# Kernel optimization log

Hardware: AMD Instinct MI355X
Metric: run time of the kernel (lower is better)

Reference implementation:

```python
import jax, jax.numpy as jnp
import numpy as np

N = 100000
E = 1600000
H = 128
IN = 16
OUT = 16
L = 3
G = 256  # number of graphs
EPS = 1e-12


def setup_inputs() -> dict:
    key = jax.random.key(0)
    ks = jax.random.split(key, 24)
    s = 0.05
    inp = {
        "x": jax.random.normal(ks[0], (N, IN), jnp.float32),
        "pos": jax.random.normal(ks[1], (N, 3), jnp.float32),
        "edge_index": jax.random.randint(ks[2], (2, E), 0, N, jnp.int64),
        "batch": jnp.sort(jax.random.randint(ks[3], (N,), 0, G, jnp.int64)),
        # node_lin: Linear(IN,H), ReLU, Linear(H,H)
        "node_W1": jax.random.normal(ks[4], (IN, H), jnp.float32) * s,
        "node_b1": jnp.zeros((H,), jnp.float32),
        "node_W2": jax.random.normal(ks[5], (H, H), jnp.float32) * s,
        "node_b2": jnp.zeros((H,), jnp.float32),
        # per-layer local_nn: Linear(H+4,H), ReLU, Linear(H,H)  (stacked over L)
        "local_W1": jax.random.normal(ks[6], (L, H + 4, H), jnp.float32) * s,
        "local_b1": jnp.zeros((L, H), jnp.float32),
        "local_W2": jax.random.normal(ks[7], (L, H, H), jnp.float32) * s,
        "local_b2": jnp.zeros((L, H), jnp.float32),
        # per-layer global_nn: Linear(H,H), ReLU, Linear(H,H)
        "global_W1": jax.random.normal(ks[8], (L, H, H), jnp.float32) * s,
        "global_b1": jnp.zeros((L, H), jnp.float32),
        "global_W2": jax.random.normal(ks[9], (L, H, H), jnp.float32) * s,
        "global_b2": jnp.zeros((L, H), jnp.float32),
        # heads
        "lin1_W": jax.random.normal(ks[10], (H, H // 2), jnp.float32) * s,
        "lin1_b": jnp.zeros((H // 2,), jnp.float32),
        "lin2_W": jax.random.normal(ks[11], (H // 2, OUT), jnp.float32) * s,
        "lin2_b": jnp.zeros((OUT,), jnp.float32),
    }
    return inp


def _angle(v1, v2):
    c = jnp.cross(v1, v2, axis=1)
    return jnp.arctan2(jnp.linalg.norm(c, axis=1), jnp.sum(v1 * v2, axis=1))


def reference(x, pos, edge_index, batch,
              node_W1, node_b1, node_W2, node_b2,
              local_W1, local_b1, local_W2, local_b2,
              global_W1, global_b1, global_W2, global_b2,
              lin1_W, lin1_b, lin2_W, lin2_b):
    src = edge_index[0]  # j (source)
    dst = edge_index[1]  # i (target, aggregation index)

    normal = pos / (jnp.linalg.norm(pos, axis=-1, keepdims=True) + EPS)

    pos_i, pos_j = pos[dst], pos[src]
    n_i, n_j = normal[dst], normal[src]
    pseudo = pos_j - pos_i  # [E, 3]
    # point-pair features [E, 4] (constant across layers since pos is fixed)
    ppf = jnp.stack([
        jnp.linalg.norm(pseudo, axis=1),
        _angle(n_i, pseudo),
        _angle(n_j, pseudo),
        _angle(n_i, n_j),
    ], axis=1)

    # node_lin (x is 2D -> MLP path; embedding path unused)
    h = jax.nn.relu(x @ node_W1 + node_b1) @ node_W2 + node_b2  # [N, H]

    for l in range(L):
        msg = jnp.concatenate([h[src], ppf], axis=1)  # [E, H+4]
        msg = jax.nn.relu(msg @ local_W1[l] + local_b1[l]) @ local_W2[l] + local_b2[l]
        agg = jax.ops.segment_sum(msg, dst, num_segments=N)  # scatter-add to nodes
        h = jax.nn.relu(agg @ global_W1[l] + global_b1[l]) @ global_W2[l] + global_b2[l]
        h = jax.nn.relu(h)

    out = jax.nn.relu(h @ lin1_W + lin1_b) @ lin2_W + lin2_b  # [N, OUT]
    return jax.ops.segment_sum(out, batch, num_segments=G)  # [G, OUT]
```

## Files before the change

kernel.cpp:

```cpp
#include <hip/hip_runtime.h>

#define NN 100000
#define NE 1600000
#define HD 128
#define NL 3
#define NG 256
#define NB 196
#define BCAP 56

typedef __attribute__((ext_vector_type(8))) short short8;
typedef __attribute__((ext_vector_type(4))) float floatx4;

static __device__ __forceinline__ unsigned short f2bf(float f) {
    unsigned int u = __float_as_uint(f);
    u += 0x7fffu + ((u >> 16) & 1u);
    return (unsigned short)(u >> 16);
}
static __device__ __forceinline__ float bf2f(unsigned short h) {
    return __uint_as_float(((unsigned int)h) << 16);
}
static __device__ __forceinline__ float angle3(float ax, float ay, float az,
                                               float bx, float by, float bz) {
    float cx = ay*bz - az*by;
    float cy = az*bx - ax*bz;
    float cz = ax*by - ay*bx;
    float cn = sqrtf(cx*cx + cy*cy + cz*cz);
    float d  = ax*bx + ay*by + az*bz;
    return atan2f(cn, d);
}


struct PrepSrcs { const float* p[14]; };

__global__ void k_prep(PrepSrcs s, unsigned short* __restrict__ dst) {
    int mat = blockIdx.y;
    int N = (mat == 13) ? 64 : 128;
    int e = blockIdx.x * 256 + threadIdx.x;
    if (e >= N * 128) return;
    int n = e >> 7, k = e & 127;
    dst[mat * 16384 + n * 128 + k] = f2bf(s.p[mat][k * N + n]);
}


__global__ void k_pn(const float* __restrict__ pos, float4* __restrict__ pn, int n) {
    int i = blockIdx.x * blockDim.x + threadIdx.x;
    if (i >= n) return;
    float x = pos[3*i], y = pos[3*i+1], z = pos[3*i+2];
    float inv = 1.0f / (sqrtf(x*x + y*y + z*z) + 1e-12f);
    pn[2*i]   = make_float4(x, y, z, 0.0f);
    pn[2*i+1] = make_float4(x*inv, y*inv, z*inv, 0.0f);
}


__global__ __launch_bounds__(256) void k_bcount(const int* __restrict__ ei,
                                                int* __restrict__ bcnt, int e) {
    __shared__ int cnt[NB];
    int tid = threadIdx.x;
    for (int i = tid; i < NB; i += 256) cnt[i] = 0;
    __syncthreads();
    int i0 = blockIdx.x * 4096 + tid * 16;
    if (i0 < e) {
#pragma unroll
        for (int q = 0; q < 4; q++) {
            int4 d4 = *(const int4*)(ei + NE + i0 + q * 4);
            atomicAdd(&cnt[d4.x >> 9], 1);
            atomicAdd(&cnt[d4.y >> 9], 1);
            atomicAdd(&cnt[d4.z >> 9], 1);
            atomicAdd(&cnt[d4.w >> 9], 1);
        }
    }
    __syncthreads();
    for (int i = tid; i < NB; i += 256)
        if (cnt[i]) atomicAdd(&bcnt[i], cnt[i]);
}

__global__ void k_bscan(const int* __restrict__ bcnt, int* __restrict__ bbase,
                        int* __restrict__ bcursor, int* __restrict__ starts) {
    if (threadIdx.x == 0 && blockIdx.x == 0) {
        int acc = 0;
        for (int b = 0; b < NB; b++) {
            bbase[b] = acc; bcursor[b] = acc;
            acc += bcnt[b];
        }
        bbase[NB] = acc;
        starts[NN] = NE;
    }
}

__global__ __launch_bounds__(256) void k_bscatter(const int* __restrict__ ei,
                                                  int* __restrict__ bcursor,
                                                  unsigned int* __restrict__ bids, int e) {
    __shared__ int lcnt[NB];
    __shared__ unsigned int lbuf[NB * BCAP];
    int tid = threadIdx.x;
    for (int i = tid; i < NB; i += 256) lcnt[i] = 0;
    __syncthreads();
    int i0 = blockIdx.x * 4096 + tid * 16;
    if (i0 < e) {
#pragma unroll
        for (int q = 0; q < 4; q++) {
            int4 d4 = *(const int4*)(ei + NE + i0 + q * 4);
            int ds[4] = {d4.x, d4.y, d4.z, d4.w};
#pragma unroll
            for (int r = 0; r < 4; r++) {
                int d = ds[r];
                int b = d >> 9;
                unsigned int w = ((unsigned int)(d & 511) << 23) | (unsigned int)(i0 + q * 4 + r);
                int pos = atomicAdd(&lcnt[b], 1);
                if (pos < BCAP) lbuf[b * BCAP + pos] = w;
                else { int p = atomicAdd(&bcursor[b], 1); bids[p] = w; }
            }
        }
    }
    __syncthreads();
    if (tid < NB) {
        int c = lcnt[tid];
        if (c > BCAP) c = BCAP;
        if (c > 0) {
            int base = atomicAdd(&bcursor[tid], c);
            for (int k = 0; k < c; k++) bids[base + k] = lbuf[tid * BCAP + k];
        }
    }
}

__global__ __launch_bounds__(256) void k_bfinal(const unsigned int* __restrict__ bids,
                                                const int* __restrict__ bbase,
                                                int* __restrict__ perm,
                                                int* __restrict__ starts,
                                                int* __restrict__ deg) {
    __shared__ int s1[512];
    __shared__ int s2[256];
    int tid = threadIdx.x;
    int b = blockIdx.x;
    int node0 = b << 9;
    int base0 = bbase[b];
    int cnt = bbase[b + 1] - base0;
    s1[2 * tid] = 0; s1[2 * tid + 1] = 0;
    __syncthreads();
    for (int j = tid; j < cnt; j += 256)
        atomicAdd(&s1[bids[base0 + j] >> 23], 1);
    __syncthreads();
    int a0 = s1[2 * tid], a1 = s1[2 * tid + 1];
    s2[tid] = a0 + a1;
    __syncthreads();
    for (int off = 1; off < 256; off <<= 1) {
        int v = (tid >= off) ? s2[tid - off] : 0;
        __syncthreads();
        s2[tid] += v;
        __syncthreads();
    }
    int pairBase = (tid ? s2[tid - 1] : 0);
    int e0 = base0 + pairBase;
    int e1 = e0 + a0;
    int n0 = node0 + 2 * tid;
    if (n0 < NN)     { starts[n0] = e0;     deg[n0] = a0; }
    if (n0 + 1 < NN) { starts[n0 + 1] = e1; deg[n0 + 1] = a1; }
    s1[2 * tid] = e0; s1[2 * tid + 1] = e1;
    __syncthreads();
    for (int j = tid; j < cnt; j += 256) {
        unsigned int w = bids[base0 + j];
        int loc = w >> 23;
        int id = (int)(w & 0x7fffffu);
        int p = atomicAdd(&s1[loc], 1);
        perm[p] = id;
    }
}

__global__ void k_ppf_sorted(const int* __restrict__ perm, const int* __restrict__ ei,
                             const float4* __restrict__ pn,
                             int* __restrict__ ssrc, float4* __restrict__ sppf, int e) {
    int j = blockIdx.x * blockDim.x + threadIdx.x;
    if (j >= e) return;
    int i = perm[j];
    int s = ei[i];
    int d = ei[NE + i];
    float4 ps_ = pn[2*s], ns_ = pn[2*s+1];
    float4 pd_ = pn[2*d], nd_ = pn[2*d+1];
    float px = ps_.x - pd_.x;
    float py = ps_.y - pd_.y;
    float pz = ps_.z - pd_.z;
    float f0 = sqrtf(px*px + py*py + pz*pz);
    float f1 = angle3(nd_.x, nd_.y, nd_.z, px, py, pz);
    float f2 = angle3(ns_.x, ns_.y, ns_.z, px, py, pz);
    float f3 = angle3(nd_.x, nd_.y, nd_.z, ns_.x, ns_.y, ns_.z);
    ssrc[j] = s;
    sppf[j] = make_float4(f0, f1, f2, f3);
}


__global__ void k_node_lin1(const float* __restrict__ x, const float* __restrict__ W1,
                            const float* __restrict__ b1, unsigned short* __restrict__ u, int n) {
    __shared__ float sW[16 * HD];
    __shared__ float sb[HD];
    __shared__ float sx[16 * 16];
    int tid = threadIdx.x;
    for (int idx = tid; idx < 16 * HD; idx += 256) sW[idx] = W1[idx];
    if (tid < HD) sb[tid] = b1[tid];
    int r0 = blockIdx.x * 16;
    for (int idx = tid; idx < 16 * 16; idx += 256) {
        int r = r0 + (idx >> 4);
        sx[idx] = (r < n) ? x[r * 16 + (idx & 15)] : 0.0f;
    }
    __syncthreads();
    int col = tid & 127;
    int rsub = tid >> 7;
    float wcol[16];
#pragma unroll
    for (int k = 0; k < 16; k++) wcol[k] = sW[k * HD + col];
    float bb = sb[col];
    for (int rr = rsub; rr < 16; rr += 2) {
        int r = r0 + rr;
        if (r >= n) break;
        float acc = bb;
#pragma unroll
        for (int k = 0; k < 16; k++) acc = fmaf(sx[rr * 16 + k], wcol[k], acc);
        u[r * HD + col] = f2bf(fmaxf(acc, 0.0f));
    }
}


template <int NC, int EPI>
__global__ __launch_bounds__(256, 2) void k_gemm128(
    const unsigned short* __restrict__ A, const unsigned short* __restrict__ Wt,
    const float* __restrict__ bias, const int* __restrict__ deg,
    const float* __restrict__ b2, unsigned short* __restrict__ out, int n) {
    constexpr int SK = 136;
    __shared__ unsigned short Bt[NC * SK];
    int tid = threadIdx.x;
    for (int idx = tid; idx < NC * 16; idx += 256) {
        int c = idx >> 4, k8 = idx & 15;
        *(short8*)&Bt[c * SK + k8 * 8] = ((const short8*)Wt)[idx];
    }
    __syncthreads();

    int wave = tid >> 6, lane = tid & 63;
    int quad = lane >> 4, m = lane & 15;
    int rowBase = blockIdx.x * 128 + wave * 32;

    short8 a[2][4];
#pragma unroll
    for (int rt = 0; rt < 2; rt++) {
        int r = rowBase + rt * 16 + m;
        int rc = (r < n) ? r : (n - 1);
        const unsigned short* ap = A + (size_t)rc * 128 + quad * 8;
#pragma unroll
        for (int s = 0; s < 4; s++) a[rt][s] = *(const short8*)(ap + s * 32);
    }

    constexpr int NT = NC / 16;
    floatx4 acc[2][NT];
    floatx4 z = {0.0f, 0.0f, 0.0f, 0.0f};
#pragma unroll
    for (int rt = 0; rt < 2; rt++)
#pragma unroll
        for (int ct = 0; ct < NT; ct++) acc[rt][ct] = z;

#pragma unroll
    for (int ct = 0; ct < NT; ct++) {
        const unsigned short* bp = &Bt[(ct * 16 + m) * SK + quad * 8];
#pragma unroll
        for (int s = 0; s < 4; s++) {
            short8 b = *(const short8*)(bp + s * 32);
            acc[0][ct] = __builtin_amdgcn_mfma_f32_16x16x32_bf16(a[0][s], b, acc[0][ct], 0, 0, 0);
            acc[1][ct] = __builtin_amdgcn_mfma_f32_16x16x32_bf16(a[1][s], b, acc[1][ct], 0, 0, 0);
        }
    }

    float dv[2][4];
    if (EPI == 2) {
#pragma unroll
        for (int rt = 0; rt < 2; rt++)
#pragma unroll
            for (int r = 0; r < 4; r++) {
                int orow = rowBase + rt * 16 + quad * 4 + r;
                dv[rt][r] = (orow < n) ? (float)deg[orow] : 0.0f;
            }
    }

#pragma unroll
    for (int ct = 0; ct < NT; ct++) {
        int col = ct * 16 + m;
        float bv = (EPI == 0) ? 0.0f : ((EPI == 2) ? b2[col] : bias[col]);
#pragma unroll
        for (int rt = 0; rt < 2; rt++) {
#pragma unroll
            for (int r = 0; r < 4; r++) {
                int orow = rowBase + rt * 16 + quad * 4 + r;
                if (orow < n) {
                    float v = acc[rt][ct][r];
                    if (EPI == 1 || EPI == 3) v += bv;
                    if (EPI == 2) v += dv[rt][r] * bv;
                    if (EPI == 3) v = fmaxf(v, 0.0f);
                    out[(size_t)orow * NC + col] = f2bf(v);
                }
            }
        }
    }
}


#define SKW 136
#define SKT 136

__global__ __launch_bounds__(256) void k_gchain(
    const unsigned short* __restrict__ S, const unsigned short* __restrict__ W2t,
    const unsigned short* __restrict__ GW1t, const unsigned short* __restrict__ GW2t,
    const int* __restrict__ deg, const float* __restrict__ b2,
    const float* __restrict__ Gb1, const float* __restrict__ Gb2,
    unsigned short* __restrict__ out, int n) {
    __shared__ unsigned short LW[128 * SKW];
    __shared__ unsigned short LT[64 * SKT];
    __shared__ float sb2[128], sg1[128], sg2[128];
    int tid = threadIdx.x;
    if (tid < 128) { sb2[tid] = b2[tid]; sg1[tid] = Gb1[tid]; sg2[tid] = Gb2[tid]; }
    for (int idx = tid; idx < 128 * 16; idx += 256) {
        int c = idx >> 4, k8 = idx & 15;
        *(short8*)&LW[c * SKW + k8 * 8] = ((const short8*)W2t)[idx];
    }
    int wave = tid >> 6, lane = tid & 63, quad = lane >> 4, m = lane & 15;
    int rowA = blockIdx.x * 64 + wave * 16 + m;
    int rcA = rowA < n ? rowA : n - 1;
    short8 a[4];
    {
        const unsigned short* ap = S + (size_t)rcA * 128 + quad * 8;
#pragma unroll
        for (int s = 0; s < 4; s++) a[s] = *(const short8*)(ap + s * 32);
    }
    __syncthreads();

    floatx4 acc[8];
    floatx4 z = {0.0f, 0.0f, 0.0f, 0.0f};
#pragma unroll
    for (int ct = 0; ct < 8; ct++) acc[ct] = z;
#pragma unroll
    for (int ct = 0; ct < 8; ct++) {
        const unsigned short* bp = &LW[(ct * 16 + m) * SKW + quad * 8];
#pragma unroll
        for (int s = 0; s < 4; s++) {
            short8 b = *(const short8*)(bp + s * 32);
            acc[ct] = __builtin_amdgcn_mfma_f32_16x16x32_bf16(a[s], b, acc[ct], 0, 0, 0);
        }
    }
    int rowC = wave * 16 + quad * 4;
    float dv[4];
#pragma unroll
    for (int r = 0; r < 4; r++) {
        int gr = blockIdx.x * 64 + rowC + r;
        dv[r] = (float)deg[gr < n ? gr : n - 1];
    }
#pragma unroll
    for (int ct = 0; ct < 8; ct++) {
        int col = ct * 16 + m;
        float bb = sb2[col];
#pragma unroll
        for (int r = 0; r < 4; r++)
            LT[(rowC + r) * SKT + col] = f2bf(acc[ct][r] + dv[r] * bb);
    }
    __syncthreads();

    for (int idx = tid; idx < 128 * 16; idx += 256) {
        int c = idx >> 4, k8 = idx & 15;
        *(short8*)&LW[c * SKW + k8 * 8] = ((const short8*)GW1t)[idx];
    }
    {
        const unsigned short* tp = &LT[(wave * 16 + m) * SKT + quad * 8];
#pragma unroll
        for (int s = 0; s < 4; s++) a[s] = *(const short8*)(tp + s * 32);
    }
    __syncthreads();

#pragma unroll
    for (int ct = 0; ct < 8; ct++) acc[ct] = z;
#pragma unroll
    for (int ct = 0; ct < 8; ct++) {
        const unsigned short* bp = &LW[(ct * 16 + m) * SKW + quad * 8];
#pragma unroll
        for (int s = 0; s < 4; s++) {
            short8 b = *(const short8*)(bp + s * 32);
            acc[ct] = __builtin_amdgcn_mfma_f32_16x16x32_bf16(a[s], b, acc[ct], 0, 0, 0);
        }
    }
#pragma unroll
    for (int ct = 0; ct < 8; ct++) {
        int col = ct * 16 + m;
        float bb = sg1[col];
#pragma unroll
        for (int r = 0; r < 4; r++)
            LT[(rowC + r) * SKT + col] = f2bf(fmaxf(acc[ct][r] + bb, 0.0f));
    }
    __syncthreads();

    for (int idx = tid; idx < 128 * 16; idx += 256) {
        int c = idx >> 4, k8 = idx & 15;
        *(short8*)&LW[c * SKW + k8 * 8] = ((const short8*)GW2t)[idx];
    }
    {
        const unsigned short* tp = &LT[(wave * 16 + m) * SKT + quad * 8];
#pragma unroll
        for (int s = 0; s < 4; s++) a[s] = *(const short8*)(tp + s * 32);
    }
    __syncthreads();

#pragma unroll
    for (int ct = 0; ct < 8; ct++) acc[ct] = z;
#pragma unroll
    for (int ct = 0; ct < 8; ct++) {
        const unsigned short* bp = &LW[(ct * 16 + m) * SKW + quad * 8];
#pragma unroll
        for (int s = 0; s < 4; s++) {
            short8 b = *(const short8*)(bp + s * 32);
            acc[ct] = __builtin_amdgcn_mfma_f32_16x16x32_bf16(a[s], b, acc[ct], 0, 0, 0);
        }
    }
#pragma unroll
    for (int ct = 0; ct < 8; ct++) {
        int col = ct * 16 + m;
        float bb = sg2[col];
#pragma unroll
        for (int r = 0; r < 4; r++) {
            int gr = blockIdx.x * 64 + rowC + r;
            if (gr < n) out[(size_t)gr * 128 + col] = f2bf(fmaxf(acc[ct][r] + bb, 0.0f));
        }
    }
}


static __device__ __forceinline__ void agg_edge(unsigned int u, float4 p,
                                                float2 w0, float2 w1, float2 w2, float2 w3,
                                                float2 bb, float& a0, float& a1) {
    float tlo = __uint_as_float(u << 16);
    float thi = __uint_as_float(u & 0xffff0000u);
    float g0 = fmaf(p.x, w0.x, fmaf(p.y, w1.x, fmaf(p.z, w2.x, fmaf(p.w, w3.x, bb.x + tlo))));
    float g1 = fmaf(p.x, w0.y, fmaf(p.y, w1.y, fmaf(p.z, w2.y, fmaf(p.w, w3.y, bb.y + thi))));
    a0 += fmaxf(g0, 0.0f);
    a1 += fmaxf(g1, 0.0f);
}

__global__ __launch_bounds__(256, 8) void k_agg(
    const int* __restrict__ starts, const int* __restrict__ ssrc,
    const float4* __restrict__ sppf, const unsigned int* __restrict__ t,
    const float* __restrict__ W1p, const float* __restrict__ b1,
    unsigned int* __restrict__ S, int n) {
    int node = (blockIdx.x * 256 + threadIdx.x) >> 6;
    if (node >= n) return;
    int lane = threadIdx.x & 63;
    int c2 = lane * 2;
    float2 w0 = *(const float2*)(W1p + c2);
    float2 w1 = *(const float2*)(W1p + 128 + c2);
    float2 w2 = *(const float2*)(W1p + 256 + c2);
    float2 w3 = *(const float2*)(W1p + 384 + c2);
    float2 bb = *(const float2*)(b1 + c2);
    int e0 = __builtin_amdgcn_readfirstlane(starts[node]);
    int e1 = __builtin_amdgcn_readfirstlane(starts[node + 1]);
    float a0 = 0.0f, a1 = 0.0f;
    int e = e0;
    for (; e + 4 <= e1; e += 4) {
        int s0 = ssrc[e], s1 = ssrc[e + 1], s2 = ssrc[e + 2], s3 = ssrc[e + 3];
        float4 p0 = sppf[e], p1 = sppf[e + 1], p2 = sppf[e + 2], p3 = sppf[e + 3];
        unsigned int u0 = t[(size_t)s0 * 64 + lane];
        unsigned int u1 = t[(size_t)s1 * 64 + lane];
        unsigned int u2 = t[(size_t)s2 * 64 + lane];
        unsigned int u3 = t[(size_t)s3 * 64 + lane];
        agg_edge(u0, p0, w0, w1, w2, w3, bb, a0, a1);
        agg_edge(u1, p1, w0, w1, w2, w3, bb, a0, a1);
        agg_edge(u2, p2, w0, w1, w2, w3, bb, a0, a1);
        agg_edge(u3, p3, w0, w1, w2, w3, bb, a0, a1);
    }
    for (; e < e1; e++) {
        int s0 = ssrc[e];
        float4 p0 = sppf[e];
        unsigned int u0 = t[(size_t)s0 * 64 + lane];
        agg_edge(u0, p0, w0, w1, w2, w3, bb, a0, a1);
    }
    unsigned int r = ((unsigned int)f2bf(a1) << 16) | f2bf(a0);
    S[(size_t)node * 64 + lane] = r;
}


__global__ void k_head2(const unsigned short* __restrict__ v, const float* __restrict__ W,
                        const float* __restrict__ b, const int* __restrict__ batch,
                        float* __restrict__ outg, int n) {
    __shared__ float sW[64 * 16];
    __shared__ float sb[16];
    __shared__ float sacc[64][17];
    __shared__ int sbid[64];
    int tid = threadIdx.x;
    for (int idx = tid; idx < 64 * 16; idx += 256) sW[idx] = W[idx];
    if (tid < 16) sb[tid] = b[tid];
    int r0 = blockIdx.x * 64;
    if (tid < 64) {
        int r = r0 + tid;
        sbid[tid] = (r < n) ? batch[r] : -1;
    }
    __syncthreads();
    int rl = tid >> 4, c = tid & 15;
#pragma unroll
    for (int i = 0; i < 4; i++) {
        int row = rl + i * 16;
        int r = r0 + row;
        float acc = 0.0f;
        if (r < n) {
            const unsigned int* vr = (const unsigned int*)(v + (size_t)r * 64);
            acc = sb[c];
#pragma unroll
            for (int k2 = 0; k2 < 32; k2++) {
                unsigned int u = vr[k2];
                acc = fmaf(__uint_as_float(u << 16), sW[(2 * k2) * 16 + c], acc);
                acc = fmaf(__uint_as_float(u & 0xffff0000u), sW[(2 * k2 + 1) * 16 + c], acc);
            }
        }
        sacc[row][c] = acc;
    }
    __syncthreads();
    if (tid < 16) {
        int cc = tid;
        float run = 0.0f;
        int cur = sbid[0];
        for (int row = 0; row < 64; row++) {
            int bid = sbid[row];
            if (bid != cur) {
                if (cur >= 0) atomicAdd(&outg[cur * 16 + cc], run);
                run = 0.0f;
                cur = bid;
            }
            run += sacc[row][cc];
        }
        if (cur >= 0) atomicAdd(&outg[cur * 16 + cc], run);
    }
}


extern "C" void kernel_launch(void* const* d_in, const int* in_sizes, int n_in,
                              void* d_out, int out_size, void* d_ws, size_t ws_size,
                              hipStream_t stream) {
    (void)in_sizes; (void)n_in; (void)out_size; (void)ws_size;
    const float* x    = (const float*)d_in[0];
    const float* pos  = (const float*)d_in[1];
    const int*   ei   = (const int*)d_in[2];
    const int*   batch= (const int*)d_in[3];
    const float* nW1  = (const float*)d_in[4];
    const float* nb1  = (const float*)d_in[5];
    const float* nW2  = (const float*)d_in[6];
    const float* nb2  = (const float*)d_in[7];
    const float* lW1  = (const float*)d_in[8];
    const float* lb1  = (const float*)d_in[9];
    const float* lW2  = (const float*)d_in[10];
    const float* lb2  = (const float*)d_in[11];
    const float* gW1  = (const float*)d_in[12];
    const float* gb1  = (const float*)d_in[13];
    const float* gW2  = (const float*)d_in[14];
    const float* gb2  = (const float*)d_in[15];
    const float* l1W  = (const float*)d_in[16];
    const float* l1b  = (const float*)d_in[17];
    const float* l2W  = (const float*)d_in[18];
    const float* l2b  = (const float*)d_in[19];
    float* outg = (float*)d_out;

    char* ws = (char*)d_ws;
    size_t off = 0;
    auto alloc = [&](size_t bytes) -> void* {
        void* p = ws + off;
        off = (off + bytes + 255) & ~(size_t)255;
        return p;
    };
    unsigned short* P0 = (unsigned short*)alloc((size_t)NN * HD * 2);
    unsigned short* P1 = (unsigned short*)alloc((size_t)NN * HD * 2);
    float4* sppf = (float4*)alloc((size_t)NE * 16);
    int* ssrc    = (int*)alloc((size_t)NE * 4);
    float4* pn   = (float4*)alloc((size_t)NN * 32);
    int* deg     = (int*)alloc((size_t)NN * 4);
    int* starts  = (int*)alloc((size_t)(NN + 2) * 4);
    int* bcnt    = (int*)alloc((size_t)(NB + 2) * 4);
    int* bbase   = (int*)alloc((size_t)(NB + 2) * 4);
    int* bcursor = (int*)alloc((size_t)(NB + 2) * 4);
    unsigned short* pw = (unsigned short*)alloc((size_t)14 * 16384 * 2);
    int* perm          = (int*)P0;
    unsigned int* bids = (unsigned int*)((char*)P0 + ((size_t)NE * 4 + 256));

    PrepSrcs ps;
    ps.p[0] = nW2;
    for (int l = 0; l < 3; l++) {
        ps.p[1 + l] = lW1 + (size_t)l * 132 * 128;
        ps.p[4 + l] = lW2 + (size_t)l * 16384;
        ps.p[7 + l] = gW1 + (size_t)l * 16384;
        ps.p[10 + l] = gW2 + (size_t)l * 16384;
    }
    ps.p[13] = l1W;

    hipMemsetAsync(bcnt, 0, (size_t)(NB + 2) * 4, stream);
    hipMemsetAsync(outg, 0, (size_t)NG * 16 * 4, stream);

    k_prep<<<dim3(64, 14), 256, 0, stream>>>(ps, pw);
    k_pn<<<(NN + 255) / 256, 256, 0, stream>>>(pos, pn, NN);
    const int NTILE = (NE + 4095) / 4096;
    k_bcount<<<NTILE, 256, 0, stream>>>(ei, bcnt, NE);
    k_bscan<<<1, 64, 0, stream>>>(bcnt, bbase, bcursor, starts);
    k_bscatter<<<NTILE, 256, 0, stream>>>(ei, bcursor, bids, NE);
    k_bfinal<<<NB, 256, 0, stream>>>(bids, bbase, perm, starts, deg);
    k_ppf_sorted<<<(NE + 255) / 256, 256, 0, stream>>>(perm, ei, pn, ssrc, sppf, NE);

    k_node_lin1<<<(NN + 15) / 16, 256, 0, stream>>>(x, nW1, nb1, P1, NN);
    const int GB = (NN + 127) / 128;
    k_gemm128<128, 1><<<GB, 256, 0, stream>>>(P1, pw, nb2, nullptr, nullptr, P0, NN);

    unsigned short* hbuf = P0;
    unsigned short* obuf = P1;
    const int AGB = (NN * 64 + 255) / 256;
    const int CGB = (NN + 63) / 64;
    for (int l = 0; l < NL; l++) {
        const float* W1p = lW1 + (size_t)l * 132 * 128 + 128 * 128;
        const float* b1  = lb1 + l * 128;
        const float* b2  = lb2 + l * 128;
        const float* Gb1 = gb1 + l * 128;
        const float* Gb2 = gb2 + l * 128;
        const unsigned short* pwW1h = pw + (size_t)(1 + l) * 16384;
        const unsigned short* pwW2  = pw + (size_t)(4 + l) * 16384;
        const unsigned short* pwGW1 = pw + (size_t)(7 + l) * 16384;
        const unsigned short* pwGW2 = pw + (size_t)(10 + l) * 16384;
        k_gemm128<128, 0><<<GB, 256, 0, stream>>>(hbuf, pwW1h, nullptr, nullptr, nullptr, obuf, NN);
        k_agg<<<AGB, 256, 0, stream>>>(starts, ssrc, sppf, (const unsigned int*)obuf,
                                       W1p, b1, (unsigned int*)hbuf, NN);
        k_gchain<<<CGB, 256, 0, stream>>>(hbuf, pwW2, pwGW1, pwGW2, deg, b2, Gb1, Gb2, obuf, NN);
        unsigned short* tmp = hbuf; hbuf = obuf; obuf = tmp;
    }
    k_gemm128<64, 3><<<GB, 256, 0, stream>>>(hbuf, pw + (size_t)13 * 16384, l1b,
                                             nullptr, nullptr, obuf, NN);
    k_head2<<<(NN + 63) / 64, 256, 0, stream>>>(obuf, l2W, l2b, batch, outg, NN);
}
```

Before: 616.2 us.

## Fuse per-layer GEMM chains into one kernel and pack PPF features as bf16

```diff
diff --git a/kernel.cpp b/kernel.cpp
--- a/kernel.cpp
+++ b/kernel.cpp
@@ -168,7 +168,7 @@
 
 __global__ void k_ppf_sorted(const int* __restrict__ perm, const int* __restrict__ ei,
                              const float4* __restrict__ pn,
-                             int* __restrict__ ssrc, float4* __restrict__ sppf, int e) {
+                             int* __restrict__ ssrc, uint2* __restrict__ sppf, int e) {
     int j = blockIdx.x * blockDim.x + threadIdx.x;
     if (j >= e) return;
     int i = perm[j];
@@ -184,7 +184,10 @@
     float f2 = angle3(ns_.x, ns_.y, ns_.z, px, py, pz);
     float f3 = angle3(nd_.x, nd_.y, nd_.z, ns_.x, ns_.y, ns_.z);
     ssrc[j] = s;
-    sppf[j] = make_float4(f0, f1, f2, f3);
+    uint2 w;
+    w.x = ((unsigned int)f2bf(f1) << 16) | f2bf(f0);
+    w.y = ((unsigned int)f2bf(f3) << 16) | f2bf(f2);
+    sppf[j] = w;
 }
 
 
@@ -219,208 +222,89 @@
 }
 
 
-template <int NC, int EPI>
-__global__ __launch_bounds__(256, 2) void k_gemm128(
-    const unsigned short* __restrict__ A, const unsigned short* __restrict__ Wt,
-    const float* __restrict__ bias, const int* __restrict__ deg,
-    const float* __restrict__ b2, unsigned short* __restrict__ out, int n) {
-    constexpr int SK = 136;
-    __shared__ unsigned short Bt[NC * SK];
+#define SKW 136
+#define SKT 136
+
+struct ChainArgs {
+    const unsigned short* W[4];
+    const float* bias[4];
+    int epi[4];
+};
+
+template <int NS, int NCL>
+__global__ __launch_bounds__(256) void k_chain(
+    const unsigned short* __restrict__ in, ChainArgs ca,
+    const int* __restrict__ deg, unsigned short* __restrict__ out, int n) {
+    __shared__ unsigned short LW[128 * SKW];
+    __shared__ unsigned short LT[64 * SKT];
     int tid = threadIdx.x;
-    for (int idx = tid; idx < NC * 16; idx += 256) {
-        int c = idx >> 4, k8 = idx & 15;
-        *(short8*)&Bt[c * SK + k8 * 8] = ((const short8*)Wt)[idx];
-    }
-    __syncthreads();
-
-    int wave = tid >> 6, lane = tid & 63;
-    int quad = lane >> 4, m = lane & 15;
-    int rowBase = blockIdx.x * 128 + wave * 32;
-
-    short8 a[2][4];
-#pragma unroll
-    for (int rt = 0; rt < 2; rt++) {
-        int r = rowBase + rt * 16 + m;
-        int rc = (r < n) ? r : (n - 1);
-        const unsigned short* ap = A + (size_t)rc * 128 + quad * 8;
-#pragma unroll
-        for (int s = 0; s < 4; s++) a[rt][s] = *(const short8*)(ap + s * 32);
-    }
-
-    constexpr int NT = NC / 16;
-    floatx4 acc[2][NT];
+    int wave = tid >> 6, lane = tid & 63, quad = lane >> 4, m = lane & 15;
+    int rowC = wave * 16 + quad * 4;
     floatx4 z = {0.0f, 0.0f, 0.0f, 0.0f};
-#pragma unroll
-    for (int rt = 0; rt < 2; rt++)
-#pragma unroll
-        for (int ct = 0; ct < NT; ct++) acc[rt][ct] = z;
-
-#pragma unroll
-    for (int ct = 0; ct < NT; ct++) {
-        const unsigned short* bp = &Bt[(ct * 16 + m) * SK + quad * 8];
-#pragma unroll
-        for (int s = 0; s < 4; s++) {
-            short8 b = *(const short8*)(bp + s * 32);
-            acc[0][ct] = __builtin_amdgcn_mfma_f32_16x16x32_bf16(a[0][s], b, acc[0][ct], 0, 0, 0);
-            acc[1][ct] = __builtin_amdgcn_mfma_f32_16x16x32_bf16(a[1][s], b, acc[1][ct], 0, 0, 0);
-        }
-    }
-
-    float dv[2][4];
-    if (EPI == 2) {
-#pragma unroll
-        for (int rt = 0; rt < 2; rt++)
+    short8 a[4];
+    {
+        int rowA = blockIdx.x * 64 + wave * 16 + m;
+        int rcA = rowA < n ? rowA : n - 1;
+        const unsigned short* ap = in + (size_t)rcA * 128 + quad * 8;
+#pragma unroll
+        for (int s = 0; s < 4; s++) a[s] = *(const short8*)(ap + s * 32);
+    }
+#pragma unroll
+    for (int st = 0; st < NS; st++) {
+        const int NC = (st == NS - 1) ? NCL : 128;
+        for (int idx = tid; idx < NC * 16; idx += 256) {
+            int c = idx >> 4, k8 = idx & 15;
+            *(short8*)&LW[c * SKW + k8 * 8] = ((const short8*)ca.W[st])[idx];
+        }
+        if (st > 0) {
+            const unsigned short* tp = &LT[(wave * 16 + m) * SKT + quad * 8];
+#pragma unroll
+            for (int s = 0; s < 4; s++) a[s] = *(const short8*)(tp + s * 32);
+        }
+        __syncthreads();
+
+        floatx4 acc[8];
+#pragma unroll
+        for (int ct = 0; ct < 8; ct++) acc[ct] = z;
+#pragma unroll
+        for (int ct = 0; ct < NC / 16; ct++) {
+            const unsigned short* bp = &LW[(ct * 16 + m) * SKW + quad * 8];
+#pragma unroll
+            for (int s = 0; s < 4; s++) {
+                short8 b = *(const short8*)(bp + s * 32);
+                acc[ct] = __builtin_amdgcn_mfma_f32_16x16x32_bf16(a[s], b, acc[ct], 0, 0, 0);
+            }
+        }
+        int epi = ca.epi[st];
+        const float* bptr = ca.bias[st];
+        float dv[4];
+        if (epi == 2) {
 #pragma unroll
             for (int r = 0; r < 4; r++) {
-                int orow = rowBase + rt * 16 + quad * 4 + r;
-                dv[rt][r] = (orow < n) ? (float)deg[orow] : 0.0f;
+                int gr = blockIdx.x * 64 + rowC + r;
+                dv[r] = (float)deg[gr < n ? gr : n - 1];
             }
-    }
-
-#pragma unroll
-    for (int ct = 0; ct < NT; ct++) {
-        int col = ct * 16 + m;
-        float bv = (EPI == 0) ? 0.0f : ((EPI == 2) ? b2[col] : bias[col]);
-#pragma unroll
-        for (int rt = 0; rt < 2; rt++) {
+        }
+#pragma unroll
+        for (int ct = 0; ct < NC / 16; ct++) {
+            int col = ct * 16 + m;
+            float bv = epi ? bptr[col] : 0.0f;
 #pragma unroll
             for (int r = 0; r < 4; r++) {
-                int orow = rowBase + rt * 16 + quad * 4 + r;
-                if (orow < n) {
-                    float v = acc[rt][ct][r];
-                    if (EPI == 1 || EPI == 3) v += bv;
-                    if (EPI == 2) v += dv[rt][r] * bv;
-                    if (EPI == 3) v = fmaxf(v, 0.0f);
-                    out[(size_t)orow * NC + col] = f2bf(v);
+                float v = acc[ct][r];
+                if (epi == 1 || epi == 3) v += bv;
+                if (epi == 2) v += dv[r] * bv;
+                if (epi == 3) v = fmaxf(v, 0.0f);
+                unsigned short bw = f2bf(v);
+                if (st == NS - 1) {
+                    int gr = blockIdx.x * 64 + rowC + r;
+                    if (gr < n) out[(size_t)gr * NCL + col] = bw;
+                } else {
+                    LT[(rowC + r) * SKT + col] = bw;
                 }
             }
         }
-    }
-}
-
-
-#define SKW 136
-#define SKT 136
-
-__global__ __launch_bounds__(256) void k_gchain(
-    const unsigned short* __restrict__ S, const unsigned short* __restrict__ W2t,
-    const unsigned short* __restrict__ GW1t, const unsigned short* __restrict__ GW2t,
-    const int* __restrict__ deg, const float* __restrict__ b2,
-    const float* __restrict__ Gb1, const float* __restrict__ Gb2,
-    unsigned short* __restrict__ out, int n) {
-    __shared__ unsigned short LW[128 * SKW];
-    __shared__ unsigned short LT[64 * SKT];
-    __shared__ float sb2[128], sg1[128], sg2[128];
-    int tid = threadIdx.x;
-    if (tid < 128) { sb2[tid] = b2[tid]; sg1[tid] = Gb1[tid]; sg2[tid] = Gb2[tid]; }
-    for (int idx = tid; idx < 128 * 16; idx += 256) {
-        int c = idx >> 4, k8 = idx & 15;
-        *(short8*)&LW[c * SKW + k8 * 8] = ((const short8*)W2t)[idx];
-    }
-    int wave = tid >> 6, lane = tid & 63, quad = lane >> 4, m = lane & 15;
-    int rowA = blockIdx.x * 64 + wave * 16 + m;
-    int rcA = rowA < n ? rowA : n - 1;
-    short8 a[4];
-    {
-        const unsigned short* ap = S + (size_t)rcA * 128 + quad * 8;
-#pragma unroll
-        for (int s = 0; s < 4; s++) a[s] = *(const short8*)(ap + s * 32);
-    }
-    __syncthreads();
-
-    floatx4 acc[8];
-    floatx4 z = {0.0f, 0.0f, 0.0f, 0.0f};
-#pragma unroll
-    for (int ct = 0; ct < 8; ct++) acc[ct] = z;
-#pragma unroll
-    for (int ct = 0; ct < 8; ct++) {
-        const unsigned short* bp = &LW[(ct * 16 + m) * SKW + quad * 8];
-#pragma unroll
-        for (int s = 0; s < 4; s++) {
-            short8 b = *(const short8*)(bp + s * 32);
-            acc[ct] = __builtin_amdgcn_mfma_f32_16x16x32_bf16(a[s], b, acc[ct], 0, 0, 0);
-        }
-    }
-    int rowC = wave * 16 + quad * 4;
-    float dv[4];
-#pragma unroll
-    for (int r = 0; r < 4; r++) {
-        int gr = blockIdx.x * 64 + rowC + r;
-        dv[r] = (float)deg[gr < n ? gr : n - 1];
-    }
-#pragma unroll
-    for (int ct = 0; ct < 8; ct++) {
-        int col = ct * 16 + m;
-        float bb = sb2[col];
-#pragma unroll
-        for (int r = 0; r < 4; r++)
-            LT[(rowC + r) * SKT + col] = f2bf(acc[ct][r] + dv[r] * bb);
-    }
-    __syncthreads();
-
-    for (int idx = tid; idx < 128 * 16; idx += 256) {
-        int c = idx >> 4, k8 = idx & 15;
-        *(short8*)&LW[c * SKW + k8 * 8] = ((const short8*)GW1t)[idx];
-    }
-    {
-        const unsigned short* tp = &LT[(wave * 16 + m) * SKT + quad * 8];
-#pragma unroll
-        for (int s = 0; s < 4; s++) a[s] = *(const short8*)(tp + s * 32);
-    }
-    __syncthreads();
-
-#pragma unroll
-    for (int ct = 0; ct < 8; ct++) acc[ct] = z;
-#pragma unroll
-    for (int ct = 0; ct < 8; ct++) {
-        const unsigned short* bp = &LW[(ct * 16 + m) * SKW + quad * 8];
-#pragma unroll
-        for (int s = 0; s < 4; s++) {
-            short8 b = *(const short8*)(bp + s * 32);
-            acc[ct] = __builtin_amdgcn_mfma_f32_16x16x32_bf16(a[s], b, acc[ct], 0, 0, 0);
-        }
-    }
-#pragma unroll
-    for (int ct = 0; ct < 8; ct++) {
-        int col = ct * 16 + m;
-        float bb = sg1[col];
-#pragma unroll
-        for (int r = 0; r < 4; r++)
-            LT[(rowC + r) * SKT + col] = f2bf(fmaxf(acc[ct][r] + bb, 0.0f));
-    }
-    __syncthreads();
-
-    for (int idx = tid; idx < 128 * 16; idx += 256) {
-        int c = idx >> 4, k8 = idx & 15;
-        *(short8*)&LW[c * SKW + k8 * 8] = ((const short8*)GW2t)[idx];
-    }
-    {
-        const unsigned short* tp = &LT[(wave * 16 + m) * SKT + quad * 8];
-#pragma unroll
-        for (int s = 0; s < 4; s++) a[s] = *(const short8*)(tp + s * 32);
-    }
-    __syncthreads();
-
-#pragma unroll
-    for (int ct = 0; ct < 8; ct++) acc[ct] = z;
-#pragma unroll
-    for (int ct = 0; ct < 8; ct++) {
-        const unsigned short* bp = &LW[(ct * 16 + m) * SKW + quad * 8];
-#pragma unroll
-        for (int s = 0; s < 4; s++) {
-            short8 b = *(const short8*)(bp + s * 32);
-            acc[ct] = __builtin_amdgcn_mfma_f32_16x16x32_bf16(a[s], b, acc[ct], 0, 0, 0);
-        }
-    }
-#pragma unroll
-    for (int ct = 0; ct < 8; ct++) {
-        int col = ct * 16 + m;
-        float bb = sg2[col];
-#pragma unroll
-        for (int r = 0; r < 4; r++) {
-            int gr = blockIdx.x * 64 + rowC + r;
-            if (gr < n) out[(size_t)gr * 128 + col] = f2bf(fmaxf(acc[ct][r] + bb, 0.0f));
-        }
+        __syncthreads();
     }
 }
 
@@ -436,9 +320,18 @@
     a1 += fmaxf(g1, 0.0f);
 }
 
+static __device__ __forceinline__ float4 unpack_ppf(uint2 w) {
+    float4 p;
+    p.x = __uint_as_float(w.x << 16);
+    p.y = __uint_as_float(w.x & 0xffff0000u);
+    p.z = __uint_as_float(w.y << 16);
+    p.w = __uint_as_float(w.y & 0xffff0000u);
+    return p;
+}
+
 __global__ __launch_bounds__(256, 8) void k_agg(
     const int* __restrict__ starts, const int* __restrict__ ssrc,
-    const float4* __restrict__ sppf, const unsigned int* __restrict__ t,
+    const uint2* __restrict__ sppf, const unsigned int* __restrict__ t,
     const float* __restrict__ W1p, const float* __restrict__ b1,
     unsigned int* __restrict__ S, int n) {
     int node = (blockIdx.x * 256 + threadIdx.x) >> 6;
@@ -456,21 +349,21 @@
     int e = e0;
     for (; e + 4 <= e1; e += 4) {
         int s0 = ssrc[e], s1 = ssrc[e + 1], s2 = ssrc[e + 2], s3 = ssrc[e + 3];
-        float4 p0 = sppf[e], p1 = sppf[e + 1], p2 = sppf[e + 2], p3 = sppf[e + 3];
+        uint2 q0 = sppf[e], q1 = sppf[e + 1], q2 = sppf[e + 2], q3 = sppf[e + 3];
         unsigned int u0 = t[(size_t)s0 * 64 + lane];
         unsigned int u1 = t[(size_t)s1 * 64 + lane];
         unsigned int u2 = t[(size_t)s2 * 64 + lane];
         unsigned int u3 = t[(size_t)s3 * 64 + lane];
-        agg_edge(u0, p0, w0, w1, w2, w3, bb, a0, a1);
-        agg_edge(u1, p1, w0, w1, w2, w3, bb, a0, a1);
-        agg_edge(u2, p2, w0, w1, w2, w3, bb, a0, a1);
-        agg_edge(u3, p3, w0, w1, w2, w3, bb, a0, a1);
+        agg_edge(u0, unpack_ppf(q0), w0, w1, w2, w3, bb, a0, a1);
+        agg_edge(u1, unpack_ppf(q1), w0, w1, w2, w3, bb, a0, a1);
+        agg_edge(u2, unpack_ppf(q2), w0, w1, w2, w3, bb, a0, a1);
+        agg_edge(u3, unpack_ppf(q3), w0, w1, w2, w3, bb, a0, a1);
     }
     for (; e < e1; e++) {
         int s0 = ssrc[e];
-        float4 p0 = sppf[e];
+        uint2 q0 = sppf[e];
         unsigned int u0 = t[(size_t)s0 * 64 + lane];
-        agg_edge(u0, p0, w0, w1, w2, w3, bb, a0, a1);
+        agg_edge(u0, unpack_ppf(q0), w0, w1, w2, w3, bb, a0, a1);
     }
     unsigned int r = ((unsigned int)f2bf(a1) << 16) | f2bf(a0);
     S[(size_t)node * 64 + lane] = r;
@@ -565,7 +458,7 @@
     };
     unsigned short* P0 = (unsigned short*)alloc((size_t)NN * HD * 2);
     unsigned short* P1 = (unsigned short*)alloc((size_t)NN * HD * 2);
-    float4* sppf = (float4*)alloc((size_t)NE * 16);
+    uint2* sppf  = (uint2*)alloc((size_t)NE * 8);
     int* ssrc    = (int*)alloc((size_t)NE * 4);
     float4* pn   = (float4*)alloc((size_t)NN * 32);
     int* deg     = (int*)alloc((size_t)NN * 4);
@@ -600,30 +493,39 @@
     k_ppf_sorted<<<(NE + 255) / 256, 256, 0, stream>>>(perm, ei, pn, ssrc, sppf, NE);
 
     k_node_lin1<<<(NN + 15) / 16, 256, 0, stream>>>(x, nW1, nb1, P1, NN);
-    const int GB = (NN + 127) / 128;
-    k_gemm128<128, 1><<<GB, 256, 0, stream>>>(P1, pw, nb2, nullptr, nullptr, P0, NN);
-
-    unsigned short* hbuf = P0;
-    unsigned short* obuf = P1;
+
+    const int CGB = (NN + 63) / 64;
     const int AGB = (NN * 64 + 255) / 256;
-    const int CGB = (NN + 63) / 64;
+
+    {
+        ChainArgs ca;
+        ca.W[0] = pw;                       ca.bias[0] = nb2;     ca.epi[0] = 1;
+        ca.W[1] = pw + (size_t)1 * 16384;   ca.bias[1] = nullptr; ca.epi[1] = 0;
+        ca.W[2] = nullptr; ca.bias[2] = nullptr; ca.epi[2] = 0;
+        ca.W[3] = nullptr; ca.bias[3] = nullptr; ca.epi[3] = 0;
+        k_chain<2, 128><<<CGB, 256, 0, stream>>>(P1, ca, deg, P0, NN);
+    }
+
+    unsigned short* tbuf = P0;
+    unsigned short* sbuf = P1;
     for (int l = 0; l < NL; l++) {
         const float* W1p = lW1 + (size_t)l * 132 * 128 + 128 * 128;
         const float* b1  = lb1 + l * 128;
-        const float* b2  = lb2 + l * 128;
-        const float* Gb1 = gb1 + l * 128;
-        const float* Gb2 = gb2 + l * 128;
-        const unsigned short* pwW1h = pw + (size_t)(1 + l) * 16384;
-        const unsigned short* pwW2  = pw + (size_t)(4 + l) * 16384;
-        const unsigned short* pwGW1 = pw + (size_t)(7 + l) * 16384;
-        const unsigned short* pwGW2 = pw + (size_t)(10 + l) * 16384;
-        k_gemm128<128, 0><<<GB, 256, 0, stream>>>(hbuf, pwW1h, nullptr, nullptr, nullptr, obuf, NN);
-        k_agg<<<AGB, 256, 0, stream>>>(starts, ssrc, sppf, (const unsigned int*)obuf,
-                                       W1p, b1, (unsigned int*)hbuf, NN);
-        k_gchain<<<CGB, 256, 0, stream>>>(hbuf, pwW2, pwGW1, pwGW2, deg, b2, Gb1, Gb2, obuf, NN);
-        unsigned short* tmp = hbuf; hbuf = obuf; obuf = tmp;
-    }
-    k_gemm128<64, 3><<<GB, 256, 0, stream>>>(hbuf, pw + (size_t)13 * 16384, l1b,
-                                             nullptr, nullptr, obuf, NN);
-    k_head2<<<(NN + 63) / 64, 256, 0, stream>>>(obuf, l2W, l2b, batch, outg, NN);
-}
+        k_agg<<<AGB, 256, 0, stream>>>(starts, ssrc, sppf, (const unsigned int*)tbuf,
+                                       W1p, b1, (unsigned int*)sbuf, NN);
+        ChainArgs ca;
+        ca.W[0] = pw + (size_t)(4 + l) * 16384;  ca.bias[0] = lb2 + l * 128; ca.epi[0] = 2;
+        ca.W[1] = pw + (size_t)(7 + l) * 16384;  ca.bias[1] = gb1 + l * 128; ca.epi[1] = 3;
+        ca.W[2] = pw + (size_t)(10 + l) * 16384; ca.bias[2] = gb2 + l * 128; ca.epi[2] = 3;
+        if (l < NL - 1) {
+            ca.W[3] = pw + (size_t)(2 + l) * 16384;
+            ca.bias[3] = nullptr; ca.epi[3] = 0;
+            k_chain<4, 128><<<CGB, 256, 0, stream>>>(sbuf, ca, deg, tbuf, NN);
+        } else {
+            ca.W[3] = pw + (size_t)13 * 16384;
+            ca.bias[3] = l1b; ca.epi[3] = 3;
+            k_chain<4, 64><<<CGB, 256, 0, stream>>>(sbuf, ca, deg, tbuf, NN);
+        }
+    }
+    k_head2<<<(NN + 63) / 64, 256, 0, stream>>>(tbuf, l2W, l2b, batch, outg, NN);
+}
```

Result: slower. 674.5 us (+9.5%).
